# Optimization experiments

Measured on AMD Instinct MI355X. Metric: run time of the kernel, lower is better.

## Reference

```python
import jax, jax.numpy as jnp
import numpy as np

N = 98304   # nodes
E = 393216  # directed edges (avg degree 4)
B = 4096    # graphs


def setup_inputs() -> dict:
    key = jax.random.key(0)
    ks = iter(jax.random.split(key, 40))
    rn = lambda shape, s=0.05: jax.random.normal(next(ks), shape, jnp.float32) * s
    inp = {
        'x': jax.random.normal(next(ks), (N, 78), jnp.float32),
        'edge_index': jax.random.randint(next(ks), (2, E), 0, N, jnp.int32),
        # sorted graph assignment covering all B graphs (~24 nodes each)
        'batch': ((jnp.arange(N, dtype=jnp.int32) * B) // N).astype(jnp.int32),
        'target': jax.random.normal(next(ks), (B, 800), jnp.float32),
        'fingerprint': jax.random.normal(next(ks), (B, 167), jnp.float32),
        # GCN layers (PyG GCNConv: transform then sym-normalized aggregate)
        'W1': rn((78, 78)), 'b1': jnp.zeros((78,), jnp.float32),
        'W2': rn((78, 156)), 'b2': jnp.zeros((156,), jnp.float32),
        'W3': rn((156, 312)), 'b3': jnp.zeros((312,), jnp.float32),
        'Wg1': rn((312, 1024)), 'bg1': jnp.zeros((1024,), jnp.float32),
        'Wg2': rn((1024, 128)), 'bg2': jnp.zeros((128,), jnp.float32),
        'Wd': rn((800, 512)), 'bd': jnp.zeros((512,), jnp.float32),
        'Wd2': rn((512, 256)), 'bd2': jnp.zeros((256,), jnp.float32),
        'Wd3': rn((256, 128)), 'bd3': jnp.zeros((128,), jnp.float32),
        'Wfp': rn((167, 128)), 'bfp': jnp.zeros((128,), jnp.float32),
        'Wf1': rn((256, 1024)), 'bf1': jnp.zeros((1024,), jnp.float32),
        'Wf2': rn((1024, 512)), 'bf2': jnp.zeros((512,), jnp.float32),
        'Wo': rn((512, 1)), 'bo': jnp.zeros((1,), jnp.float32),
    }
    return inp


def reference(x, edge_index, batch, target, fingerprint,
              W1, b1, W2, b2, W3, b3, Wg1, bg1, Wg2, bg2,
              Wd, bd, Wd2, bd2, Wd3, bd3, Wfp, bfp,
              Wf1, bf1, Wf2, bf2, Wo, bo):
    src, dst = edge_index[0], edge_index[1]
    loop = jnp.arange(N, dtype=src.dtype)
    s = jnp.concatenate([src, loop])  # with self-loops
    d = jnp.concatenate([dst, loop])
    deg = jax.ops.segment_sum(jnp.ones(s.shape[0], jnp.float32), d, num_segments=N)
    dinv = jnp.where(deg > 0, jax.lax.rsqrt(deg), 0.0)
    norm = (dinv[s] * dinv[d])[:, None]  # [E+N, 1]

    def gcn(h, W, b):
        h = h @ W  # transform first (PyG GCNConv)
        msg = h[s] * norm  # gather + scale
        return jax.ops.segment_sum(msg, d, num_segments=N) + b

    h = jax.nn.relu(gcn(x, W1, b1))
    h = jax.nn.relu(gcn(h, W2, b2))
    h = jax.nn.relu(gcn(h, W3, b3))
    g = jax.ops.segment_max(h, batch, num_segments=B)  # global max pool [B, 312]
    g = jax.nn.relu(g @ Wg1 + bg1)
    g = g @ Wg2 + bg2  # dropout is identity in eval

    xt = jax.nn.relu(target @ Wd + bd)
    xt = jax.nn.relu(xt @ Wd2 + bd2)
    xt = xt @ Wd3 + bd3

    fp = fingerprint @ Wfp + bfp  # computed but unused, faithful to source
    del fp

    xc = jnp.concatenate([g, xt], axis=1)  # [B, 256]
    xc = jax.nn.relu(xc @ Wf1 + bf1)
    xc = jax.nn.relu(xc @ Wf2 + bf2)
    return xc @ Wo + bo  # [B, 1]
```

## Files before the change

### kernel.cpp

```cpp
#include <hip/hip_runtime.h>

static constexpr int NNODE = 98304;
static constexpr int NEDGE = 393216;
static constexpr int NB    = 4096;
static constexpr int CAP   = 32;

typedef __attribute__((ext_vector_type(8))) short  short8;
typedef __attribute__((ext_vector_type(8))) unsigned short ushort8;
typedef __attribute__((ext_vector_type(4))) float  f32x4;

__device__ inline unsigned short f2bf(float x) {
    unsigned int u = __float_as_uint(x);
    u += 0x7fffu + ((u >> 16) & 1u);
    return (unsigned short)(u >> 16);
}
__device__ inline float bf2f(unsigned short h) {
    return __uint_as_float(((unsigned int)h) << 16);
}

static constexpr int OW1 = 0,         NW1 = 128 * 96;
static constexpr int OW2 = OW1 + NW1, NW2 = 192 * 96;
static constexpr int OW3 = OW2 + NW2, NW3 = 320 * 160;
static constexpr int OG1 = OW3 + NW3, NG1 = 1024 * 320;
static constexpr int OG2 = OG1 + NG1, NG2 = 128 * 1024;
static constexpr int OD1 = OG2 + NG2, ND1 = 512 * 800;
static constexpr int OD2 = OD1 + ND1, ND2 = 256 * 512;
static constexpr int OD3 = OD2 + ND2, ND3 = 128 * 256;
static constexpr int OF1 = OD3 + ND3, NF1 = 1024 * 256;
static constexpr int OF2 = OF1 + NF1, NF2 = 512 * 1024;
static constexpr int WTOT = OF2 + NF2;


__global__ void k_zeroi(int* p, int n) {
    int i = blockIdx.x * blockDim.x + threadIdx.x;
    if (i < n) p[i] = 0;
}
__global__ void k_fillv(float* p, float v, int n) {
    int i = blockIdx.x * blockDim.x + threadIdx.x;
    if (i < n) p[i] = v;
}
__global__ void k_counti(const int* __restrict__ dst, int* cnt, int e) {
    int i = blockIdx.x * blockDim.x + threadIdx.x;
    if (i < e) atomicAdd(&cnt[dst[i]], 1);
}
__global__ void k_dinv(const int* __restrict__ cnt, float* dinv, int n) {
    int i = blockIdx.x * blockDim.x + threadIdx.x;
    if (i < n) dinv[i] = rsqrtf(1.0f + (float)cnt[i]);
}
__global__ void k_bucket(const int* __restrict__ src, const int* __restrict__ dst,
                         const float* __restrict__ dinv, int* pos,
                         int* __restrict__ bsrc, float* __restrict__ bnrm, int e) {
    int i = blockIdx.x * blockDim.x + threadIdx.x;
    if (i >= e) return;
    int s = src[i], d = dst[i];
    int p = atomicAdd(&pos[d], 1);
    if (p < CAP) {
        bsrc[(size_t)d * CAP + p] = s;
        bnrm[(size_t)d * CAP + p] = dinv[s] * dinv[d];
    }
}
__global__ void k_sortbk(const int* __restrict__ cnt, int* __restrict__ bsrc,
                         float* __restrict__ bnrm, int n) {
    int node = blockIdx.x * blockDim.x + threadIdx.x;
    if (node >= n) return;
    int deg = min(cnt[node], CAP);
    size_t base = (size_t)node * CAP;
    for (int i = 1; i < deg; ++i) {
        int s = bsrc[base + i];
        float v = bnrm[base + i];
        int j = i - 1;
        while (j >= 0 && bsrc[base + j] > s) {
            bsrc[base + j + 1] = bsrc[base + j];
            bnrm[base + j + 1] = bnrm[base + j];
            --j;
        }
        bsrc[base + j + 1] = s;
        bnrm[base + j + 1] = v;
    }
}

struct SJob  { const float* src; int K, N, Npad, K32, off; };
struct SJobs { SJob j[10]; };

__global__ void k_splitw(SJobs js, unsigned short* __restrict__ WH,
                         unsigned short* __restrict__ WL) {
    int tid = blockIdx.x * blockDim.x + threadIdx.x;
    int stride = gridDim.x * blockDim.x;
    #pragma unroll 1
    for (int w = 0; w < 10; ++w) {
        SJob jb = js.j[w];
        int tot = jb.Npad * jb.K32;
        for (int i = tid; i < tot; i += stride) {
            int n = i / jb.K32, k = i - n * jb.K32;
            float x = (k < jb.K && n < jb.N) ? jb.src[(size_t)k * jb.N + n] : 0.0f;
            unsigned short h = f2bf(x);
            WH[jb.off + i] = h;
            WL[jb.off + i] = f2bf(x - bf2f(h));
        }
    }
}

template<int DIM, int KS>
__global__ void k_gather_sp(const float* __restrict__ t, const int* __restrict__ cnt,
                            const int* __restrict__ bsrc, const float* __restrict__ bnrm,
                            const float* __restrict__ dinv,
                            unsigned short* __restrict__ Ph,
                            unsigned short* __restrict__ Pl, int n) {
    constexpr int H = KS / 2;
    int i = blockIdx.x * blockDim.x + threadIdx.x;
    if (i >= n * H) return;
    int node = i / H;
    int c2 = (i - node * H) * 2;
    size_t o = (size_t)node * KS + c2;
    if (c2 >= DIM) {
        *(unsigned int*)&Ph[o] = 0u;
        *(unsigned int*)&Pl[o] = 0u;
        return;
    }
    float di = dinv[node];
    float2 tv = *(const float2*)&t[(size_t)node * DIM + c2];
    float sx = tv.x * di * di, sy = tv.y * di * di;
    int deg = min(cnt[node], CAP);
    size_t base = (size_t)node * CAP;
    for (int j = 0; j < deg; ++j) {
        int s = bsrc[base + j];
        float nrm = bnrm[base + j];
        float2 v = *(const float2*)&t[(size_t)s * DIM + c2];
        sx += v.x * nrm;
        sy += v.y * nrm;
    }
    unsigned short hx = f2bf(sx), hy = f2bf(sy);
    unsigned short lx = f2bf(sx - bf2f(hx)), ly = f2bf(sy - bf2f(hy));
    *(unsigned int*)&Ph[o] = (unsigned int)hx | ((unsigned int)hy << 16);
    *(unsigned int*)&Pl[o] = (unsigned int)lx | ((unsigned int)ly << 16);
}

template<int NT, bool POOL>
__global__ __launch_bounds__(512)
void k_gemm_nres(const unsigned short* __restrict__ Ahg, const unsigned short* __restrict__ Alg,
                 const unsigned short* __restrict__ Wth, const unsigned short* __restrict__ Wtl,
                 const float* __restrict__ bias, const int* __restrict__ batch,
                 float* __restrict__ C, int M, int N, int Kb, int ldc) {
    __shared__ __align__(16) unsigned char smraw[(1 + NT) * 10240];
    ushort (*Ah)[40] = (ushort(*)[40])(smraw);
    ushort (*Al)[40] = (ushort(*)[40])(smraw + 5120);
    ushort (*Bh)[40] = (ushort(*)[40])(smraw + 10240);
    ushort (*Bl)[40] = (ushort(*)[40])(smraw + 10240 + NT * 5120);
    __shared__ int sb[64];

    const int tid  = threadIdx.x;
    const int lane = tid & 63;
    const int wv = tid >> 6;
    const int wr = wv >> 2, wc = wv & 3;
    const int m16 = lane & 15, kg = lane >> 4;
    const int row0 = blockIdx.x * 64;

    if (POOL && tid < 64) sb[tid] = batch[row0 + tid];

    f32x4 acc[NT][2];
    #pragma unroll
    for (int ct = 0; ct < NT; ++ct)
        #pragma unroll
        for (int i = 0; i < 2; ++i)
            acc[ct][i] = f32x4{0.f, 0.f, 0.f, 0.f};

    for (int k0 = 0; k0 < Kb; k0 += 32) {
        {
            int c = tid & 255;
            int row = c >> 2, ko = (c & 3) << 3;
            size_t ao = (size_t)(row0 + row) * Kb + k0 + ko;
            const unsigned short* sp = (tid < 256) ? Ahg : Alg;
            ushort (*dp)[40] = (tid < 256) ? Ah : Al;
            *(ushort8*)&dp[row][ko] = *(const ushort8*)&sp[ao];
        }
        #pragma unroll
        for (int r = 0; r < NT; ++r) {
            int id = r * 512 + tid;
            bool lo = id >= NT * 256;
            int cid = lo ? id - NT * 256 : id;
            int row = cid >> 2, ko = (cid & 3) << 3;
            size_t bo = (size_t)row * Kb + k0 + ko;
            const unsigned short* sp = lo ? Wtl : Wth;
            ushort (*dp)[40] = lo ? Bl : Bh;
            *(ushort8*)&dp[row][ko] = *(const ushort8*)&sp[bo];
        }
        __syncthreads();

        short8 ah[2], al[2];
        #pragma unroll
        for (int i = 0; i < 2; ++i) {
            ah[i] = *(const short8*)&Ah[wr * 32 + i * 16 + m16][kg * 8];
            al[i] = *(const short8*)&Al[wr * 32 + i * 16 + m16][kg * 8];
        }
        #pragma unroll
        for (int ct = 0; ct < NT; ++ct) {
            int c = ct * 64 + wc * 16 + m16;
            short8 bh = *(const short8*)&Bh[c][kg * 8];
            short8 bl = *(const short8*)&Bl[c][kg * 8];
            #pragma unroll
            for (int i = 0; i < 2; ++i) {
                acc[ct][i] = __builtin_amdgcn_mfma_f32_16x16x32_bf16(ah[i], bh, acc[ct][i], 0, 0, 0);
                acc[ct][i] = __builtin_amdgcn_mfma_f32_16x16x32_bf16(ah[i], bl, acc[ct][i], 0, 0, 0);
                acc[ct][i] = __builtin_amdgcn_mfma_f32_16x16x32_bf16(al[i], bh, acc[ct][i], 0, 0, 0);
            }
        }
        __syncthreads();
    }

    if (!POOL) {
        #pragma unroll
        for (int ct = 0; ct < NT; ++ct)
            #pragma unroll
            for (int i = 0; i < 2; ++i)
                #pragma unroll
                for (int r = 0; r < 4; ++r) {
                    int gr = row0 + wr * 32 + i * 16 + kg * 4 + r;
                    int gn = ct * 64 + wc * 16 + m16;
                    if (gn < N) {
                        float v = fmaxf(acc[ct][i][r] + bias[gn], 0.0f);
                        C[(size_t)gr * ldc + gn] = v;
                    }
                }
    } else {
        float (*Ts)[68] = (float(*)[68])smraw;
        #pragma unroll
        for (int ct = 0; ct < NT; ++ct) {
            __syncthreads();
            #pragma unroll
            for (int i = 0; i < 2; ++i)
                #pragma unroll
                for (int r = 0; r < 4; ++r) {
                    int lr = wr * 32 + i * 16 + kg * 4 + r;
                    int lc = wc * 16 + m16;
                    int gn = ct * 64 + lc;
                    float bv = (gn < N) ? bias[gn] : 0.0f;
                    Ts[lr][lc] = fmaxf(acc[ct][i][r] + bv, 0.0f);
                }
            __syncthreads();
            if (tid < 256) {
                int seg = tid >> 6, col = tid & 63;
                int gcol = ct * 64 + col;
                if (gcol < N) {
                    int gb = sb[0] + seg;
                    float mx = -1.0f;
                    for (int r = 0; r < 64; ++r)
                        if (sb[r] == gb) mx = fmaxf(mx, Ts[r][col]);
                    if (mx >= 0.0f)
                        atomicMax((int*)&C[(size_t)gb * N + gcol], __float_as_int(mx));
                }
            }
        }
    }
}

template<bool HAS_BIAS, bool RELU, bool ASPLIT, bool OSPLIT>
__global__ __launch_bounds__(256)
void k_gemm_head(const float* __restrict__ A,
                 const unsigned short* __restrict__ Ahg, const unsigned short* __restrict__ Alg,
                 const unsigned short* __restrict__ Wth, const unsigned short* __restrict__ Wtl,
                 const float* __restrict__ bias, float* __restrict__ C,
                 unsigned short* __restrict__ CH, unsigned short* __restrict__ CL,
                 int M, int N, int K, int Kb, int ldc) {
    __shared__ __align__(16) unsigned char smraw[20480];
    ushort (*Ah)[40] = (ushort(*)[40])(smraw);
    ushort (*Al)[40] = (ushort(*)[40])(smraw + 5120);
    ushort (*Bh)[40] = (ushort(*)[40])(smraw + 10240);
    ushort (*Bl)[40] = (ushort(*)[40])(smraw + 15360);

    const int tid  = threadIdx.x;
    const int lane = tid & 63;
    const int wv = tid >> 6, wr = wv >> 1, wc = wv & 1;
    const int m16 = lane & 15, kg = lane >> 4;
    const int row0 = blockIdx.y * 64, col0 = blockIdx.x * 64;
    const int mA = tid >> 2, kqA = (tid & 3) << 3;

    f32x4 acc[2][2];
    #pragma unroll
    for (int i = 0; i < 2; ++i)
        #pragma unroll
        for (int j = 0; j < 2; ++j)
            acc[i][j] = f32x4{0.f, 0.f, 0.f, 0.f};

    for (int k0 = 0; k0 < Kb; k0 += 32) {
        if (ASPLIT) {
            size_t ao = (size_t)(row0 + mA) * Kb + k0 + kqA;
            *(ushort8*)&Ah[mA][kqA] = *(const ushort8*)&Ahg[ao];
            *(ushort8*)&Al[mA][kqA] = *(const ushort8*)&Alg[ao];
        } else {
            int gr = row0 + mA;
            const float* ap = A + (size_t)gr * K + k0 + kqA;
            ushort8 vh, vl;
            #pragma unroll
            for (int u = 0; u < 8; ++u) {
                float xv = (gr < M && (k0 + kqA + u) < K) ? ap[u] : 0.f;
                unsigned short h = f2bf(xv);
                vh[u] = h; vl[u] = f2bf(xv - bf2f(h));
            }
            *(ushort8*)&Ah[mA][kqA] = vh;
            *(ushort8*)&Al[mA][kqA] = vl;
        }
        {
            int gn = col0 + mA;
            if (gn < N) {
                size_t bo = (size_t)gn * Kb + k0 + kqA;
                *(ushort8*)&Bh[mA][kqA] = *(const ushort8*)&Wth[bo];
                *(ushort8*)&Bl[mA][kqA] = *(const ushort8*)&Wtl[bo];
            } else {
                ushort8 z = {0, 0, 0, 0, 0, 0, 0, 0};
                *(ushort8*)&Bh[mA][kqA] = z;
                *(ushort8*)&Bl[mA][kqA] = z;
            }
        }
        __syncthreads();

        short8 ah[2], al[2], bh[2], bl[2];
        #pragma unroll
        for (int i = 0; i < 2; ++i) {
            ah[i] = *(const short8*)&Ah[wr * 32 + i * 16 + m16][kg * 8];
            al[i] = *(const short8*)&Al[wr * 32 + i * 16 + m16][kg * 8];
            bh[i] = *(const short8*)&Bh[wc * 32 + i * 16 + m16][kg * 8];
            bl[i] = *(const short8*)&Bl[wc * 32 + i * 16 + m16][kg * 8];
        }
        #pragma unroll
        for (int i = 0; i < 2; ++i)
            #pragma unroll
            for (int j = 0; j < 2; ++j) {
                acc[i][j] = __builtin_amdgcn_mfma_f32_16x16x32_bf16(ah[i], bh[j], acc[i][j], 0, 0, 0);
                acc[i][j] = __builtin_amdgcn_mfma_f32_16x16x32_bf16(ah[i], bl[j], acc[i][j], 0, 0, 0);
                acc[i][j] = __builtin_amdgcn_mfma_f32_16x16x32_bf16(al[i], bh[j], acc[i][j], 0, 0, 0);
            }
        __syncthreads();
    }

    #pragma unroll
    for (int i = 0; i < 2; ++i)
        #pragma unroll
        for (int r = 0; r < 4; ++r) {
            int gr = row0 + wr * 32 + i * 16 + kg * 4 + r;
            if (gr >= M) continue;
            #pragma unroll
            for (int j = 0; j < 2; ++j) {
                int gn = col0 + wc * 32 + j * 16 + m16;
                if (gn >= N) continue;
                float v = acc[i][j][r];
                if (HAS_BIAS) v += bias[gn];
                if (RELU) v = fmaxf(v, 0.0f);
                if (OSPLIT) {
                    unsigned short h = f2bf(v);
                    CH[(size_t)gr * ldc + gn] = h;
                    CL[(size_t)gr * ldc + gn] = f2bf(v - bf2f(h));
                } else {
                    C[(size_t)gr * ldc + gn] = v;
                }
            }
        }
}

__global__ __launch_bounds__(256)
void k_rowdot(const float* __restrict__ A, const float* __restrict__ w,
              const float* __restrict__ b, float* __restrict__ out, int M, int K) {
    int wave = (blockIdx.x * blockDim.x + threadIdx.x) >> 6;
    int lane = threadIdx.x & 63;
    if (wave >= M) return;
    const float* row = A + (size_t)wave * K;
    float s = 0.0f;
    for (int k = lane; k < K; k += 64) s += row[k] * w[k];
    #pragma unroll
    for (int off = 32; off > 0; off >>= 1) s += __shfl_down(s, off, 64);
    if (lane == 0) out[wave] = s + b[0];
}


extern "C" void kernel_launch(void* const* d_in, const int* in_sizes, int n_in,
                              void* d_out, int out_size, void* d_ws, size_t ws_size,
                              hipStream_t stream) {
    const float* x      = (const float*)d_in[0];
    const int*   ei     = (const int*)d_in[1];
    const int*   batch  = (const int*)d_in[2];
    const float* target = (const float*)d_in[3];
    const float* W1  = (const float*)d_in[5],  *b1  = (const float*)d_in[6];
    const float* W2  = (const float*)d_in[7],  *b2  = (const float*)d_in[8];
    const float* W3  = (const float*)d_in[9],  *b3  = (const float*)d_in[10];
    const float* Wg1 = (const float*)d_in[11], *bg1 = (const float*)d_in[12];
    const float* Wg2 = (const float*)d_in[13], *bg2 = (const float*)d_in[14];
    const float* Wd  = (const float*)d_in[15], *bd  = (const float*)d_in[16];
    const float* Wd2 = (const float*)d_in[17], *bd2 = (const float*)d_in[18];
    const float* Wd3 = (const float*)d_in[19], *bd3 = (const float*)d_in[20];
    const float* Wf1 = (const float*)d_in[23], *bf1 = (const float*)d_in[24];
    const float* Wf2 = (const float*)d_in[25], *bf2 = (const float*)d_in[26];
    const float* Wo  = (const float*)d_in[27], *bo  = (const float*)d_in[28];
    float* out = (float*)d_out;

    const int* src = ei;
    const int* dst = ei + NEDGE;

    char* pb = (char*)d_ws;
    auto alloc = [&](size_t bytes) { char* r = pb; pb += (bytes + 255) & ~(size_t)255; return r; };
    float* dinv = (float*)alloc((size_t)NNODE * 4);
    int*   cnt  = (int*)  alloc((size_t)NNODE * 4);
    int*   pos  = (int*)  alloc((size_t)NNODE * 4);
    int*   bsrc = (int*)  alloc((size_t)NNODE * CAP * 4);
    float* bnrm = (float*)alloc((size_t)NNODE * CAP * 4);
    unsigned short* WH = (unsigned short*)alloc((size_t)WTOT * 2);
    unsigned short* WL = (unsigned short*)alloc((size_t)WTOT * 2);
    unsigned short* Ph = (unsigned short*)alloc((size_t)NNODE * 160 * 2);
    unsigned short* Pl = (unsigned short*)alloc((size_t)NNODE * 160 * 2);
    float* Q = (float*)alloc((size_t)NNODE * 156 * 4);

    float* gpool = Q;
    unsigned short* g1H  = (unsigned short*)(gpool + (size_t)NB * 312);
    unsigned short* g1L  = g1H  + (size_t)NB * 1024;
    unsigned short* xcH  = g1L  + (size_t)NB * 1024;
    unsigned short* xcL  = xcH  + (size_t)NB * 256;
    unsigned short* xt1H = xcL  + (size_t)NB * 256;
    unsigned short* xt1L = xt1H + (size_t)NB * 512;
    unsigned short* xt2H = xt1L + (size_t)NB * 512;
    unsigned short* xt2L = xt2H + (size_t)NB * 256;
    unsigned short* xc1H = (unsigned short*)Ph;
    unsigned short* xc1L = xc1H + (size_t)NB * 1024;
    float* xc2 = (float*)(xc1L + (size_t)NB * 1024);

    SJobs js = {{
        { W1,   78,   78,  128,   96, OW1 },
        { W2,   78,  156,  192,   96, OW2 },
        { W3,  156,  312,  320,  160, OW3 },
        { Wg1, 312, 1024, 1024,  320, OG1 },
        { Wg2, 1024, 128,  128, 1024, OG2 },
        { Wd,  800,  512,  512,  800, OD1 },
        { Wd2, 512,  256,  256,  512, OD2 },
        { Wd3, 256,  128,  128,  256, OD3 },
        { Wf1, 256, 1024, 1024,  256, OF1 },
        { Wf2, 1024, 512,  512, 1024, OF2 },
    }};
    k_splitw<<<512, 256, 0, stream>>>(js, WH, WL);

    k_zeroi <<<(2 * NNODE + 255) / 256, 256, 0, stream>>>(cnt, 2 * NNODE);
    k_counti<<<(NEDGE + 255) / 256, 256, 0, stream>>>(dst, cnt, NEDGE);
    k_dinv  <<<(NNODE + 255) / 256, 256, 0, stream>>>(cnt, dinv, NNODE);
    k_bucket<<<(NEDGE + 255) / 256, 256, 0, stream>>>(src, dst, dinv, pos, bsrc, bnrm, NEDGE);
    k_sortbk<<<(NNODE + 255) / 256, 256, 0, stream>>>(cnt, bsrc, bnrm, NNODE);

    k_gather_sp<78, 96><<<(NNODE * 48 + 255) / 256, 256, 0, stream>>>(x, cnt, bsrc, bnrm, dinv, Ph, Pl, NNODE);
    k_gemm_nres<2, false><<<NNODE / 64, 512, 0, stream>>>(Ph, Pl, WH + OW1, WL + OW1, b1, nullptr, Q, NNODE, 78, 96, 78);

    k_gather_sp<78, 96><<<(NNODE * 48 + 255) / 256, 256, 0, stream>>>(Q, cnt, bsrc, bnrm, dinv, Ph, Pl, NNODE);
    k_gemm_nres<3, false><<<NNODE / 64, 512, 0, stream>>>(Ph, Pl, WH + OW2, WL + OW2, b2, nullptr, Q, NNODE, 156, 96, 156);

    k_gather_sp<156, 160><<<(NNODE * 80 + 255) / 256, 256, 0, stream>>>(Q, cnt, bsrc, bnrm, dinv, Ph, Pl, NNODE);
    k_fillv<<<((NB * 312) + 255) / 256, 256, 0, stream>>>(gpool, 0.0f, NB * 312);
    k_gemm_nres<5, true><<<NNODE / 64, 512, 0, stream>>>(Ph, Pl, WH + OW3, WL + OW3, b3, batch, gpool, NNODE, 312, 160, 312);

    k_gemm_head<true, true, false, true><<<dim3(16, NB / 64), 256, 0, stream>>>(
        gpool, nullptr, nullptr, WH + OG1, WL + OG1, bg1, nullptr, g1H, g1L, NB, 1024, 312, 320, 1024);
    k_gemm_head<true, false, true, true><<<dim3(2, NB / 64), 256, 0, stream>>>(
        nullptr, g1H, g1L, WH + OG2, WL + OG2, bg2, nullptr, xcH, xcL, NB, 128, 1024, 1024, 256);

    k_gemm_head<true, true, false, true><<<dim3(8, NB / 64), 256, 0, stream>>>(
        target, nullptr, nullptr, WH + OD1, WL + OD1, bd, nullptr, xt1H, xt1L, NB, 512, 800, 800, 512);
    k_gemm_head<true, true, true, true><<<dim3(4, NB / 64), 256, 0, stream>>>(
        nullptr, xt1H, xt1L, WH + OD2, WL + OD2, bd2, nullptr, xt2H, xt2L, NB, 256, 512, 512, 256);
    k_gemm_head<true, false, true, true><<<dim3(2, NB / 64), 256, 0, stream>>>(
        nullptr, xt2H, xt2L, WH + OD3, WL + OD3, bd3, nullptr, xcH + 128, xcL + 128, NB, 128, 256, 256, 256);

    k_gemm_head<true, true, true, true><<<dim3(16, NB / 64), 256, 0, stream>>>(
        nullptr, xcH, xcL, WH + OF1, WL + OF1, bf1, nullptr, xc1H, xc1L, NB, 1024, 256, 256, 1024);
    k_gemm_head<true, true, true, false><<<dim3(8, NB / 64), 256, 0, stream>>>(
        nullptr, xc1H, xc1L, WH + OF2, WL + OF2, bf2, xc2, nullptr, nullptr, NB, 512, 1024, 1024, 512);

    k_rowdot<<<(NB * 64) / 256, 256, 0, stream>>>(xc2, Wo, bo, out, NB, 512);
}
```

Baseline: 777.7 us.

## Move layer-3 GEMM with fused max-pool onto column-tiled head GEMM kernel

The third GCN layer's GEMM plus global max-pool now runs on the 64x64-tiled head GEMM kernel, with a 2D grid of 5 column tiles by 1536 row tiles, instead of the full-width 512-thread node GEMM. The fused segment-max pooling is ported into the head kernel's epilogue. The aim is more blocks and more parallelism with a smaller per-block accumulator footprint. In exchange, each A row tile is reloaded once per column tile, and pooling atomics are issued per column tile.

```diff
diff --git a/kernel.cpp b/kernel.cpp
--- a/kernel.cpp
+++ b/kernel.cpp
@@ -207,58 +207,28 @@
         __syncthreads();
     }
 
-    if (!POOL) {
-        #pragma unroll
-        for (int ct = 0; ct < NT; ++ct)
-            #pragma unroll
-            for (int i = 0; i < 2; ++i)
-                #pragma unroll
-                for (int r = 0; r < 4; ++r) {
-                    int gr = row0 + wr * 32 + i * 16 + kg * 4 + r;
-                    int gn = ct * 64 + wc * 16 + m16;
-                    if (gn < N) {
-                        float v = fmaxf(acc[ct][i][r] + bias[gn], 0.0f);
-                        C[(size_t)gr * ldc + gn] = v;
-                    }
+    #pragma unroll
+    for (int ct = 0; ct < NT; ++ct)
+        #pragma unroll
+        for (int i = 0; i < 2; ++i)
+            #pragma unroll
+            for (int r = 0; r < 4; ++r) {
+                int gr = row0 + wr * 32 + i * 16 + kg * 4 + r;
+                int gn = ct * 64 + wc * 16 + m16;
+                if (gn < N) {
+                    float v = fmaxf(acc[ct][i][r] + bias[gn], 0.0f);
+                    C[(size_t)gr * ldc + gn] = v;
                 }
-    } else {
-        float (*Ts)[68] = (float(*)[68])smraw;
-        #pragma unroll
-        for (int ct = 0; ct < NT; ++ct) {
-            __syncthreads();
-            #pragma unroll
-            for (int i = 0; i < 2; ++i)
-                #pragma unroll
-                for (int r = 0; r < 4; ++r) {
-                    int lr = wr * 32 + i * 16 + kg * 4 + r;
-                    int lc = wc * 16 + m16;
-                    int gn = ct * 64 + lc;
-                    float bv = (gn < N) ? bias[gn] : 0.0f;
-                    Ts[lr][lc] = fmaxf(acc[ct][i][r] + bv, 0.0f);
-                }
-            __syncthreads();
-            if (tid < 256) {
-                int seg = tid >> 6, col = tid & 63;
-                int gcol = ct * 64 + col;
-                if (gcol < N) {
-                    int gb = sb[0] + seg;
-                    float mx = -1.0f;
-                    for (int r = 0; r < 64; ++r)
-                        if (sb[r] == gb) mx = fmaxf(mx, Ts[r][col]);
-                    if (mx >= 0.0f)
-                        atomicMax((int*)&C[(size_t)gb * N + gcol], __float_as_int(mx));
-                }
-            }
-        }
-    }
-}
-
-template<bool HAS_BIAS, bool RELU, bool ASPLIT, bool OSPLIT>
+            }
+}
+
+template<bool HAS_BIAS, bool RELU, bool ASPLIT, bool OSPLIT, bool POOL>
 __global__ __launch_bounds__(256)
 void k_gemm_head(const float* __restrict__ A,
                  const unsigned short* __restrict__ Ahg, const unsigned short* __restrict__ Alg,
                  const unsigned short* __restrict__ Wth, const unsigned short* __restrict__ Wtl,
-                 const float* __restrict__ bias, float* __restrict__ C,
+                 const float* __restrict__ bias, const int* __restrict__ batch,
+                 float* __restrict__ C,
                  unsigned short* __restrict__ CH, unsigned short* __restrict__ CL,
                  int M, int N, int K, int Kb, int ldc) {
     __shared__ __align__(16) unsigned char smraw[20480];
@@ -266,6 +236,7 @@
     ushort (*Al)[40] = (ushort(*)[40])(smraw + 5120);
     ushort (*Bh)[40] = (ushort(*)[40])(smraw + 10240);
     ushort (*Bl)[40] = (ushort(*)[40])(smraw + 15360);
+    __shared__ int sb[64];
 
     const int tid  = threadIdx.x;
     const int lane = tid & 63;
@@ -273,6 +244,8 @@
     const int m16 = lane & 15, kg = lane >> 4;
     const int row0 = blockIdx.y * 64, col0 = blockIdx.x * 64;
     const int mA = tid >> 2, kqA = (tid & 3) << 3;
+
+    if (POOL && tid < 64) sb[tid] = batch[row0 + tid];
 
     f32x4 acc[2][2];
     #pragma unroll
@@ -332,28 +305,56 @@
         __syncthreads();
     }
 
-    #pragma unroll
-    for (int i = 0; i < 2; ++i)
-        #pragma unroll
-        for (int r = 0; r < 4; ++r) {
-            int gr = row0 + wr * 32 + i * 16 + kg * 4 + r;
-            if (gr >= M) continue;
-            #pragma unroll
-            for (int j = 0; j < 2; ++j) {
-                int gn = col0 + wc * 32 + j * 16 + m16;
-                if (gn >= N) continue;
-                float v = acc[i][j][r];
-                if (HAS_BIAS) v += bias[gn];
-                if (RELU) v = fmaxf(v, 0.0f);
-                if (OSPLIT) {
-                    unsigned short h = f2bf(v);
-                    CH[(size_t)gr * ldc + gn] = h;
-                    CL[(size_t)gr * ldc + gn] = f2bf(v - bf2f(h));
-                } else {
-                    C[(size_t)gr * ldc + gn] = v;
+    if (POOL) {
+        float (*Ts)[68] = (float(*)[68])smraw;
+        #pragma unroll
+        for (int i = 0; i < 2; ++i)
+            #pragma unroll
+            for (int r = 0; r < 4; ++r) {
+                int lr = wr * 32 + i * 16 + kg * 4 + r;
+                #pragma unroll
+                for (int j = 0; j < 2; ++j) {
+                    int lc = wc * 32 + j * 16 + m16;
+                    int gn = col0 + lc;
+                    float bv = (gn < N) ? bias[gn] : 0.0f;
+                    Ts[lr][lc] = fmaxf(acc[i][j][r] + bv, 0.0f);
                 }
             }
-        }
+        __syncthreads();
+        int seg = tid >> 6, col = tid & 63;
+        int gcol = col0 + col;
+        if (gcol < N) {
+            int gb = sb[0] + seg;
+            float mx = -1.0f;
+            for (int r = 0; r < 64; ++r)
+                if (sb[r] == gb) mx = fmaxf(mx, Ts[r][col]);
+            if (mx >= 0.0f)
+                atomicMax((int*)&C[(size_t)gb * N + gcol], __float_as_int(mx));
+        }
+    } else {
+        #pragma unroll
+        for (int i = 0; i < 2; ++i)
+            #pragma unroll
+            for (int r = 0; r < 4; ++r) {
+                int gr = row0 + wr * 32 + i * 16 + kg * 4 + r;
+                if (gr >= M) continue;
+                #pragma unroll
+                for (int j = 0; j < 2; ++j) {
+                    int gn = col0 + wc * 32 + j * 16 + m16;
+                    if (gn >= N) continue;
+                    float v = acc[i][j][r];
+                    if (HAS_BIAS) v += bias[gn];
+                    if (RELU) v = fmaxf(v, 0.0f);
+                    if (OSPLIT) {
+                        unsigned short h = f2bf(v);
+                        CH[(size_t)gr * ldc + gn] = h;
+                        CL[(size_t)gr * ldc + gn] = f2bf(v - bf2f(h));
+                    } else {
+                        C[(size_t)gr * ldc + gn] = v;
+                    }
+                }
+            }
+    }
 }
 
 __global__ __launch_bounds__(256)
@@ -448,24 +449,25 @@
 
     k_gather_sp<156, 160><<<(NNODE * 80 + 255) / 256, 256, 0, stream>>>(Q, cnt, bsrc, bnrm, dinv, Ph, Pl, NNODE);
     k_fillv<<<((NB * 312) + 255) / 256, 256, 0, stream>>>(gpool, 0.0f, NB * 312);
-    k_gemm_nres<5, true><<<NNODE / 64, 512, 0, stream>>>(Ph, Pl, WH + OW3, WL + OW3, b3, batch, gpool, NNODE, 312, 160, 312);
-
-    k_gemm_head<true, true, false, true><<<dim3(16, NB / 64), 256, 0, stream>>>(
-        gpool, nullptr, nullptr, WH + OG1, WL + OG1, bg1, nullptr, g1H, g1L, NB, 1024, 312, 320, 1024);
-    k_gemm_head<true, false, true, true><<<dim3(2, NB / 64), 256, 0, stream>>>(
-        nullptr, g1H, g1L, WH + OG2, WL + OG2, bg2, nullptr, xcH, xcL, NB, 128, 1024, 1024, 256);
-
-    k_gemm_head<true, true, false, true><<<dim3(8, NB / 64), 256, 0, stream>>>(
-        target, nullptr, nullptr, WH + OD1, WL + OD1, bd, nullptr, xt1H, xt1L, NB, 512, 800, 800, 512);
-    k_gemm_head<true, true, true, true><<<dim3(4, NB / 64), 256, 0, stream>>>(
-        nullptr, xt1H, xt1L, WH + OD2, WL + OD2, bd2, nullptr, xt2H, xt2L, NB, 256, 512, 512, 256);
-    k_gemm_head<true, false, true, true><<<dim3(2, NB / 64), 256, 0, stream>>>(
-        nullptr, xt2H, xt2L, WH + OD3, WL + OD3, bd3, nullptr, xcH + 128, xcL + 128, NB, 128, 256, 256, 256);
-
-    k_gemm_head<true, true, true, true><<<dim3(16, NB / 64), 256, 0, stream>>>(
-        nullptr, xcH, xcL, WH + OF1, WL + OF1, bf1, nullptr, xc1H, xc1L, NB, 1024, 256, 256, 1024);
-    k_gemm_head<true, true, true, false><<<dim3(8, NB / 64), 256, 0, stream>>>(
-        nullptr, xc1H, xc1L, WH + OF2, WL + OF2, bf2, xc2, nullptr, nullptr, NB, 512, 1024, 1024, 512);
+    k_gemm_head<true, true, true, false, true><<<dim3(5, NNODE / 64), 256, 0, stream>>>(
+        nullptr, Ph, Pl, WH + OW3, WL + OW3, b3, batch, gpool, nullptr, nullptr, NNODE, 312, 160, 160, 312);
+
+    k_gemm_head<true, true, false, true, false><<<dim3(16, NB / 64), 256, 0, stream>>>(
+        gpool, nullptr, nullptr, WH + OG1, WL + OG1, bg1, nullptr, nullptr, g1H, g1L, NB, 1024, 312, 320, 1024);
+    k_gemm_head<true, false, true, true, false><<<dim3(2, NB / 64), 256, 0, stream>>>(
+        nullptr, g1H, g1L, WH + OG2, WL + OG2, bg2, nullptr, nullptr, xcH, xcL, NB, 128, 1024, 1024, 256);
+
+    k_gemm_head<true, true, false, true, false><<<dim3(8, NB / 64), 256, 0, stream>>>(
+        target, nullptr, nullptr, WH + OD1, WL + OD1, bd, nullptr, nullptr, xt1H, xt1L, NB, 512, 800, 800, 512);
+    k_gemm_head<true, true, true, true, false><<<dim3(4, NB / 64), 256, 0, stream>>>(
+        nullptr, xt1H, xt1L, WH + OD2, WL + OD2, bd2, nullptr, nullptr, xt2H, xt2L, NB, 256, 512, 512, 256);
+    k_gemm_head<true, false, true, true, false><<<dim3(2, NB / 64), 256, 0, stream>>>(
+        nullptr, xt2H, xt2L, WH + OD3, WL + OD3, bd3, nullptr, nullptr, xcH + 128, xcL + 128, NB, 128, 256, 256, 256);
+
+    k_gemm_head<true, true, true, true, false><<<dim3(16, NB / 64), 256, 0, stream>>>(
+        nullptr, xcH, xcL, WH + OF1, WL + OF1, bf1, nullptr, nullptr, xc1H, xc1L, NB, 1024, 256, 256, 1024);
+    k_gemm_head<true, true, true, false, false><<<dim3(8, NB / 64), 256, 0, stream>>>(
+        nullptr, xc1H, xc1L, WH + OF2, WL + OF2, bf2, nullptr, xc2, nullptr, nullptr, NB, 512, 1024, 1024, 512);
 
     k_rowdot<<<(NB * 64) / 256, 256, 0, stream>>>(xc2, Wo, bo, out, NB, 512);
 }
```

New measurement: 764.6 us. Within noise of the previous version (-1.7%).
